# Kernel tuning notes

Hardware: AMD Instinct MI355X
Metric: run time of the kernel (lower is better)

The kernel has to match this reference:

```python
import jax, jax.numpy as jnp
import numpy as np

U, I, E = 50000, 100000, 1600000
D, H, HID, B = 64, 8, 8, 16384
ALPHA = 0.2  # leaky relu slope


def setup_inputs() -> dict:
    key = jax.random.key(0)
    ks = jax.random.split(key, 12)
    return {
        "userIdx": jax.random.randint(ks[0], (B,), 0, U),
        "itemIdx": jax.random.randint(ks[1], (B,), 0, I),
        "edge_u": jax.random.randint(ks[2], (E,), 0, U),
        "edge_i": jax.random.randint(ks[3], (E,), 0, I),
        "uEmbd": jax.random.normal(ks[4], (U, D), dtype=jnp.float32) * 0.01,
        "iEmbd": jax.random.normal(ks[5], (I, D), dtype=jnp.float32) * 0.01,
        "Wu_h": jax.random.normal(ks[6], (H, D, HID), dtype=jnp.float32) * 0.18,
        "Wi_h": jax.random.normal(ks[7], (H, D, HID), dtype=jnp.float32) * 0.18,
        "a_h": jax.random.normal(ks[8], (H, 2 * HID), dtype=jnp.float32) * 0.3,
        "Wu_out": jax.random.normal(ks[9], (H * HID, D), dtype=jnp.float32) * 0.15,
        "Wi_out": jax.random.normal(ks[10], (H * HID, D), dtype=jnp.float32) * 0.15,
        "a_out": jax.random.normal(ks[11], (2 * D,), dtype=jnp.float32) * 0.1,
    }


def _leaky(x):
    return jnp.where(x >= 0, x, ALPHA * x)


def _gat_layer(fu, fi, Wu, Wi, a, edge_u, edge_i):
    # fu:[U,in], fi:[I,in], Wu/Wi:[in,out], a:[2*out]
    u_h = fu @ Wu  # [U,out]
    i_h = fi @ Wi  # [I,out]
    out = Wu.shape[1]
    # a . cat(u_h[eu], i_h[ei]) decomposed into per-node scores then edge gather
    su = u_h @ a[:out]  # [U]
    si = i_h @ a[out:]  # [I]
    e = jnp.exp(-_leaky(su[edge_u] + si[edge_i]))  # [E]
    rowsum = jax.ops.segment_sum(e, edge_u, num_segments=U)  # [U]
    colsum = jax.ops.segment_sum(e, edge_i, num_segments=I)  # [I]
    # users aggregate items they interacted with
    agg_i = jax.ops.segment_sum(e[:, None] * i_h[edge_i], edge_u, num_segments=U)  # [U,out]
    u_p = u_h + agg_i / jnp.where(rowsum == 0, 1.0, rowsum)[:, None]
    # items aggregate users (nan from empty cols -> 0, as in original)
    agg_u = jax.ops.segment_sum(e[:, None] * u_h[edge_u], edge_i, num_segments=I)  # [I,out]
    att_u = jnp.where((colsum > 0)[:, None], agg_u / jnp.where(colsum == 0, 1.0, colsum)[:, None], 0.0)
    i_p = i_h + att_u
    return u_p, i_p


def reference(userIdx, itemIdx, edge_u, edge_i, uEmbd, iEmbd, Wu_h, Wi_h, a_h, Wu_out, Wi_out, a_out):
    # eval mode: all dropout layers are identity
    fu, fi = uEmbd, iEmbd
    head = jax.vmap(lambda Wu, Wi, a: _gat_layer(fu, fi, Wu, Wi, a, edge_u, edge_i))
    u_ps, i_ps = head(Wu_h, Wi_h, a_h)  # [H,U,HID], [H,I,HID]
    # concat=True heads: elu then concatenate along feature dim (head-major columns)
    hu = jax.nn.elu(u_ps).transpose(1, 0, 2).reshape(U, H * HID)
    hi = jax.nn.elu(i_ps).transpose(1, 0, 2).reshape(I, H * HID)
    u_p, i_p = _gat_layer(hu, hi, Wu_out, Wi_out, a_out, edge_u, edge_i)
    u_f = jax.nn.elu(u_p)  # final F.elu in SpUIGAT
    i_f = jax.nn.elu(i_p)
    return jnp.sum(u_f[userIdx] * i_f[itemIdx], axis=1)  # [B]
```

## Files before the change

### kernel.cpp

```cpp
#include <hip/hip_runtime.h>
#include <hip/hip_fp16.h>

#define U_N 50000
#define I_N 100000
#define E_N 1600000
#define B_N 16384
#define UI_N (U_N + I_N)
#define NB_U 782
#define NB_I 1563
#define NBK 586
#define CAP 10240
#define NBLD 512
#define CHUNK (E_N / NBLD)
#define COL_CAP 3300000
#define MAXACT 32768

__global__ __launch_bounds__(1024) void k_build1(
    const int* __restrict__ eu, const int* __restrict__ ei,
    int* __restrict__ bcnt, int* __restrict__ storage) {
  __shared__ int hist[NBK];
  __shared__ int lbase[NBK];
  __shared__ int loff[NBK];
  int t = threadIdx.x;
  for (int b = t; b < NBK; b += 1024) { hist[b] = 0; loff[b] = 0; }
  __syncthreads();
  int e0 = blockIdx.x * CHUNK;
  int myu[4], myi[4];
  int ne = 0;
#pragma unroll
  for (int k = 0; k < 4; k++) {
    int e = e0 + t + 1024 * k;
    if (e < e0 + CHUNK) {
      int u = eu[e], it = ei[e];
      myu[k] = u;
      myi[k] = it;
      ne = k + 1;
      atomicAdd(&hist[u >> 8], 1);
      atomicAdd(&hist[(U_N + it) >> 8], 1);
    }
  }
  __syncthreads();
  for (int b = t; b < NBK; b += 1024) {
    int h = hist[b];
    lbase[b] = h ? atomicAdd(&bcnt[b], h) : 0;
  }
  __syncthreads();
#pragma unroll
  for (int k = 0; k < 4; k++) {
    if (k < ne) {
      int u = myu[k], it = myi[k];
      int k2 = U_N + it;
      int b1 = u >> 8;
      int s1 = lbase[b1] + atomicAdd(&loff[b1], 1);
      storage[(size_t)b1 * CAP + s1] = ((u & 255) << 17) | it;
      int b2 = k2 >> 8;
      int s2 = lbase[b2] + atomicAdd(&loff[b2], 1);
      storage[(size_t)b2 * CAP + s2] = ((k2 & 255) << 17) | u;
    }
  }
}

__global__ __launch_bounds__(1024) void k_scanb(const int* __restrict__ bcnt,
                                                int* __restrict__ bbase) {
  __shared__ int sc[1024];
  int t = threadIdx.x;
  int v = (t < NBK) ? bcnt[t] : 0;
  sc[t] = v;
  __syncthreads();
  int val = v;
  for (int off = 1; off < 1024; off <<= 1) {
    int x = (t >= off) ? sc[t - off] : 0;
    __syncthreads();
    val += x;
    sc[t] = val;
    __syncthreads();
  }
  if (t < NBK) bbase[t] = val - v;
}

__global__ __launch_bounds__(256) void k_build2(const int* __restrict__ bcnt,
                                                const int* __restrict__ storage,
                                                const int* __restrict__ bbase,
                                                int* __restrict__ ptr,
                                                int* __restrict__ col) {
  __shared__ int c[256];
  __shared__ int sc[256];
  __shared__ int pb[256];
  __shared__ int cur[256];
  int b = blockIdx.x;
  int t = threadIdx.x;
  c[t] = 0;
  __syncthreads();
  int n = bcnt[b];
  const int* s = storage + (size_t)b * CAP;
  for (int i = t; i < n; i += 256) atomicAdd(&c[s[i] >> 17], 1);
  __syncthreads();
  int deg = c[t];
  sc[t] = deg;
  __syncthreads();
  int val = deg;
  for (int off = 1; off < 256; off <<= 1) {
    int x = (t >= off) ? sc[t - off] : 0;
    __syncthreads();
    val += x;
    sc[t] = val;
    __syncthreads();
  }
  int base = bbase[b];
  int myPtr = base + (val - deg);
  pb[t] = myPtr;
  cur[t] = 0;
  int node = b * 256 + t;
  if (node < UI_N) ptr[node] = myPtr;
  if (b == NBK - 1 && t == 255) ptr[UI_N] = base + val;
  __syncthreads();
  for (int i = t; i < n; i += 256) {
    int e = s[i];
    int local = e >> 17;
    int slot = pb[local] + atomicAdd(&cur[local], 1);
    col[slot] = e & 0x1FFFF;
  }
}

__global__ void k_flagc(const int* __restrict__ uIdx, const int* __restrict__ iIdx,
                        int* __restrict__ flag, int* __restrict__ list,
                        int* __restrict__ nm) {
  int b = blockIdx.x * blockDim.x + threadIdx.x;
  if (b < B_N) {
    int u = uIdx[b];
    if (atomicExch(&flag[u], 1) == 0) list[atomicAdd(nm, 1)] = u;
    int it = U_N + iIdx[b];
    if (atomicExch(&flag[it], 1) == 0) list[atomicAdd(nm, 1)] = it;
  }
}

__global__ __launch_bounds__(256) void k_mm2(
    const float* __restrict__ Xu32, const float* __restrict__ Xi32,
    const __half* __restrict__ Xu16, const __half* __restrict__ Xi16,
    const float* __restrict__ Wu, const float* __restrict__ Wi,
    const float* __restrict__ a, int layer,
    __half* __restrict__ fA_U, __half* __restrict__ fA_I,
    __half* __restrict__ s16U, __half* __restrict__ s16I) {
  __shared__ float Wl[4096];
  __shared__ float Xs[4096];
  const bool isU = blockIdx.x < NB_U;
  const int N = isU ? U_N : I_N;
  const int base = (isU ? blockIdx.x : blockIdx.x - NB_U) * 64;
  const float* W = isU ? Wu : Wi;
  __half* f16 = isU ? fA_U : fA_I;
  __half* s16 = isU ? s16U : s16I;
  const int aoff = (layer == 1) ? (isU ? 0 : 8) : (isU ? 0 : 64);
  int t = threadIdx.x;

  if (layer == 1) {
#pragma unroll
    for (int k = 0; k < 4; k++) {
      int i = t + 256 * k;
      int h = i >> 7, d = (i >> 1) & 63, half = i & 1;
      float4 v = *(const float4*)(W + h * 512 + d * 8 + half * 4);
      *(float4*)(Wl + d * 64 + h * 8 + half * 4) = v;
    }
    const float* X = isU ? Xu32 : Xi32;
#pragma unroll
    for (int k = 0; k < 4; k++) {
      int i = t + 256 * k;
      int r = i >> 4, ch = i & 15;
      int node = base + r;
      float4 v = make_float4(0.f, 0.f, 0.f, 0.f);
      if (node < N) v = *(const float4*)(X + (size_t)node * 64 + ch * 4);
      *(float4*)(Xs + r * 64 + ch * 4) = v;
    }
  } else {
#pragma unroll
    for (int k = 0; k < 4; k++) {
      int i = t + 256 * k;
      *(float4*)(Wl + i * 4) = *(const float4*)(W + i * 4);
    }
    const __half* X = isU ? Xu16 : Xi16;
#pragma unroll
    for (int k = 0; k < 4; k++) {
      int i = t + 256 * k;
      int r = i >> 4, ch = i & 15;
      int node = base + r;
      float4 v = make_float4(0.f, 0.f, 0.f, 0.f);
      if (node < N) {
        const __half2* hp = (const __half2*)(X + (size_t)node * 64 + ch * 4);
        float2 f0 = __half22float2(hp[0]);
        float2 f1 = __half22float2(hp[1]);
        v = make_float4(f0.x, f0.y, f1.x, f1.y);
      }
      *(float4*)(Xs + r * 64 + ch * 4) = v;
    }
  }
  __syncthreads();

  const int c0 = t & 31;
  const int rb = t >> 5;
  float acc0[8], acc1[8];
#pragma unroll
  for (int k = 0; k < 8; k++) { acc0[k] = 0.f; acc1[k] = 0.f; }

  for (int d0 = 0; d0 < 64; d0 += 4) {
    float2 wA = *(float2*)(Wl + (d0 + 0) * 64 + 2 * c0);
    float2 wB = *(float2*)(Wl + (d0 + 1) * 64 + 2 * c0);
    float2 wC = *(float2*)(Wl + (d0 + 2) * 64 + 2 * c0);
    float2 wD = *(float2*)(Wl + (d0 + 3) * 64 + 2 * c0);
#pragma unroll
    for (int k = 0; k < 8; k++) {
      float4 x = *(float4*)(Xs + (rb + 8 * k) * 64 + d0);
      acc0[k] += x.x * wA.x + x.y * wB.x + x.z * wC.x + x.w * wD.x;
      acc1[k] += x.x * wA.y + x.y * wB.y + x.z * wC.y + x.w * wD.y;
    }
  }

  float av0, av1;
  if (layer == 1) {
    int h = c0 >> 2, j = 2 * (c0 & 3);
    av0 = a[h * 16 + aoff + j];
    av1 = a[h * 16 + aoff + j + 1];
  } else {
    av0 = a[aoff + 2 * c0];
    av1 = a[aoff + 2 * c0 + 1];
  }
#pragma unroll
  for (int k = 0; k < 8; k++) {
    int node = base + rb + 8 * k;
    float s = acc0[k] * av0 + acc1[k] * av1;
    s += __shfl_xor(s, 1);
    s += __shfl_xor(s, 2);
    if (layer != 1) {
      s += __shfl_xor(s, 4);
      s += __shfl_xor(s, 8);
      s += __shfl_xor(s, 16);
    }
    if (node < N) {
      float2 f;
      f.x = acc0[k];
      f.y = acc1[k];
      *(__half2*)(f16 + (size_t)node * 64 + 2 * c0) = __float22half2_rn(f);
      if (layer == 1) {
        if ((c0 & 3) == 0) s16[node * 8 + (c0 >> 2)] = __float2half_rn(s);
      } else {
        if (c0 == 0) s16[node] = __float2half_rn(s);
      }
    }
  }
}

template <int LAYER>
__device__ __forceinline__ void agg_body(
    const int* __restrict__ ptr, const int* __restrict__ col,
    const __half* __restrict__ fA_U, const __half* __restrict__ fA_I,
    __half* __restrict__ fB_U, __half* __restrict__ fB_I,
    const __half* __restrict__ s16U, const __half* __restrict__ s16I,
    const int* __restrict__ list, const int* __restrict__ nm) {
  int gid = blockIdx.x * blockDim.x + threadIdx.x;
  int wv = gid >> 6;
  int l = threadIdx.x & 63;
  int half = l >> 5;
  int idx = wv * 2 + half;
  bool act = true;
  int n;
  if (LAYER == 2) {
    act = idx < *nm;
    n = act ? list[idx] : 0;
  } else {
    n = idx;
  }
  int lh = l & 31;
  int g = lh >> 3;
  int cc = lh & 7;
  bool isU = n < U_N;
  int nl = isU ? n : n - U_N;
  const char* nbrF = (const char*)(isU ? fA_I : fA_U);
  const char* nbrS = (const char*)(isU ? s16I : s16U);
  const __half* selfS = isU ? s16U : s16I;
  const __half* selfF = isU ? fA_U : fA_I;
  __half* outp = isU ? fB_U : fB_I;
  const char* colc = (const char*)col;

  int beg = ptr[n], endA = ptr[n + 1];
  int deg = act ? (endA - beg) : 0;
  unsigned coff = ((unsigned)(beg + g)) << 2;
  const unsigned begb = (unsigned)beg << 2;
  const unsigned fsh = (unsigned)cc << 4;
  const unsigned ssh = (LAYER == 1) ? ((unsigned)cc << 1) : 0u;
  float sself = (LAYER == 1) ? __half2float(selfS[(size_t)nl * 8 + cc])
                             : __half2float(selfS[nl]);
  float acc[8];
#pragma unroll
  for (int k = 0; k < 8; k++) acc[k] = 0.f;
  float wsum = 0.f;

  auto edge = [&](unsigned off) {
    int nb = *(const int*)(colc + off);
    unsigned so = (LAYER == 1) ? (((unsigned)nb << 4) + ssh) : ((unsigned)nb << 1);
    float x = sself + __half2float(*(const __half*)(nbrS + so));
    float4 r = *(const float4*)(nbrF + (((unsigned)nb << 7) + fsh));
    float w = __expf(-fmaxf(x, 0.2f * x));
    wsum += w;
    const __half* h = (const __half*)&r;
#pragma unroll
    for (int k = 0; k < 8; k++) acc[k] += w * (float)h[k];
  };
  auto edgem = [&](unsigned off, bool valid) {
    unsigned o = valid ? off : begb;
    int nb = *(const int*)(colc + o);
    unsigned so = (LAYER == 1) ? (((unsigned)nb << 4) + ssh) : ((unsigned)nb << 1);
    float x = sself + __half2float(*(const __half*)(nbrS + so));
    float4 r = *(const float4*)(nbrF + (((unsigned)nb << 7) + fsh));
    float w = valid ? __expf(-fmaxf(x, 0.2f * x)) : 0.f;
    wsum += w;
    const __half* h = (const __half*)&r;
#pragma unroll
    for (int k = 0; k < 8; k++) acc[k] += w * (float)h[k];
  };

  int q = deg >> 4;
  for (; q > 0; q--) {
    edge(coff);
    edge(coff + 16);
    edge(coff + 32);
    edge(coff + 48);
    coff += 64;
  }
  int rem = deg & 15;
  if (rem) {
    edgem(coff, g < rem);
    edgem(coff + 16, (4 + g) < rem);
    edgem(coff + 32, (8 + g) < rem);
    edgem(coff + 48, (12 + g) < rem);
  }

#pragma unroll
  for (int k = 0; k < 8; k++) {
    acc[k] += __shfl_xor(acc[k], 8);
    acc[k] += __shfl_xor(acc[k], 16);
  }
  wsum += __shfl_xor(wsum, 8);
  wsum += __shfl_xor(wsum, 16);

  if (lh < 8 && act) {
    float4 raw = *(const float4*)(selfF + (size_t)nl * 64 + cc * 8);
    const __half2* sp = (const __half2*)&raw;
    float2 s0 = __half22float2(sp[0]);
    float2 s1 = __half22float2(sp[1]);
    float2 s2 = __half22float2(sp[2]);
    float2 s3 = __half22float2(sp[3]);
    float v[8] = {s0.x, s0.y, s1.x, s1.y, s2.x, s2.y, s3.x, s3.y};
    if (deg > 0) {
      float inv = 1.f / wsum;
#pragma unroll
      for (int k = 0; k < 8; k++) v[k] += acc[k] * inv;
    }
#pragma unroll
    for (int k = 0; k < 8; k++) v[k] = (v[k] > 0.f) ? v[k] : (__expf(v[k]) - 1.f);
    __half2 o[4];
    o[0] = __floats2half2_rn(v[0], v[1]);
    o[1] = __floats2half2_rn(v[2], v[3]);
    o[2] = __floats2half2_rn(v[4], v[5]);
    o[3] = __floats2half2_rn(v[6], v[7]);
    *(float4*)(outp + (size_t)nl * 64 + cc * 8) = *(float4*)o;
  }
}

__global__ __launch_bounds__(256) void k_aggL1(
    const int* __restrict__ ptr, const int* __restrict__ col,
    const __half* __restrict__ fA_U, const __half* __restrict__ fA_I,
    __half* __restrict__ fB_U, __half* __restrict__ fB_I,
    const __half* __restrict__ s16U, const __half* __restrict__ s16I) {
  agg_body<1>(ptr, col, fA_U, fA_I, fB_U, fB_I, s16U, s16I, nullptr, nullptr);
}

__global__ __launch_bounds__(256) void k_aggL2(
    const int* __restrict__ ptr, const int* __restrict__ col,
    const __half* __restrict__ fA_U, const __half* __restrict__ fA_I,
    __half* __restrict__ fB_U, __half* __restrict__ fB_I,
    const __half* __restrict__ s2U, const __half* __restrict__ s2I,
    const int* __restrict__ list, const int* __restrict__ nm) {
  agg_body<2>(ptr, col, fA_U, fA_I, fB_U, fB_I, s2U, s2I, list, nm);
}

__global__ void k_dot(const int* __restrict__ uIdx, const int* __restrict__ iIdx,
                      const __half* __restrict__ u_f, const __half* __restrict__ i_f,
                      float* __restrict__ out) {
  int t = threadIdx.x;
  int pair = blockIdx.x * 32 + (t >> 3);
  int cc = t & 7;
  float4 ra = *(const float4*)(u_f + (size_t)uIdx[pair] * 64 + cc * 8);
  float4 rb = *(const float4*)(i_f + (size_t)iIdx[pair] * 64 + cc * 8);
  const __half* ha = (const __half*)&ra;
  const __half* hb = (const __half*)&rb;
  float v = 0.f;
#pragma unroll
  for (int k = 0; k < 8; k++) v += (float)ha[k] * (float)hb[k];
  v += __shfl_xor(v, 1);
  v += __shfl_xor(v, 2);
  v += __shfl_xor(v, 4);
  if (cc == 0) out[pair] = v;
}

extern "C" void kernel_launch(void* const* d_in, const int* in_sizes, int n_in,
                              void* d_out, int out_size, void* d_ws, size_t ws_size,
                              hipStream_t stream) {
  const int* userIdx = (const int*)d_in[0];
  const int* itemIdx = (const int*)d_in[1];
  const int* edge_u = (const int*)d_in[2];
  const int* edge_i = (const int*)d_in[3];
  const float* uEmbd = (const float*)d_in[4];
  const float* iEmbd = (const float*)d_in[5];
  const float* Wu_h = (const float*)d_in[6];
  const float* Wi_h = (const float*)d_in[7];
  const float* a_h = (const float*)d_in[8];
  const float* Wu_out = (const float*)d_in[9];
  const float* Wi_out = (const float*)d_in[10];
  const float* a_out = (const float*)d_in[11];
  float* out = (float*)d_out;

  char* w = (char*)d_ws;
  size_t off = 0;
  auto alloc = [&](size_t bytes) -> void* {
    void* p = w + off;
    off += (bytes + 511) & ~(size_t)511;
    return p;
  };
  int* bcnt = (int*)alloc((size_t)(NBK + 16 + UI_N) * 4);
  int* nm = bcnt + NBK;
  int* flag = bcnt + NBK + 16;
  int* ptr = (int*)alloc((size_t)(UI_N + 1) * 4);
  int* bbase = (int*)alloc(4096);
  int* list = (int*)alloc((size_t)MAXACT * 4);
  int* col = (int*)alloc((size_t)COL_CAP * 4);
  __half* fA_U = (__half*)alloc((size_t)U_N * 64 * 2);
  __half* fA_I = (__half*)alloc((size_t)I_N * 64 * 2);
  __half* s16U = (__half*)alloc((size_t)U_N * 8 * 2);
  __half* s16I = (__half*)alloc((size_t)I_N * 8 * 2);
  __half* s2U = (__half*)alloc((size_t)U_N * 2);
  __half* s2I = (__half*)alloc((size_t)I_N * 2);
  size_t union_off = off;
  int* storage = (int*)alloc((size_t)NBK * CAP * 4);
  size_t end_storage = off;
  off = union_off;
  __half* fB_U = (__half*)alloc((size_t)U_N * 64 * 2);
  __half* fB_I = (__half*)alloc((size_t)I_N * 64 * 2);
  if (off < end_storage) off = end_storage;

  hipMemsetAsync(bcnt, 0, (size_t)(NBK + 16 + UI_N) * 4, stream);
  k_build1<<<NBLD, 1024, 0, stream>>>(edge_u, edge_i, bcnt, storage);
  k_scanb<<<1, 1024, 0, stream>>>(bcnt, bbase);
  k_build2<<<NBK, 256, 0, stream>>>(bcnt, storage, bbase, ptr, col);
  k_flagc<<<(B_N + 255) / 256, 256, 0, stream>>>(userIdx, itemIdx, flag, list, nm);

  k_mm2<<<NB_U + NB_I, 256, 0, stream>>>(uEmbd, iEmbd, (const __half*)nullptr,
                                         (const __half*)nullptr, Wu_h, Wi_h, a_h, 1,
                                         fA_U, fA_I, s16U, s16I);
  k_aggL1<<<UI_N * 32 / 256, 256, 0, stream>>>(ptr, col, fA_U, fA_I, fB_U, fB_I,
                                               s16U, s16I);

  k_mm2<<<NB_U + NB_I, 256, 0, stream>>>((const float*)nullptr, (const float*)nullptr,
                                         fB_U, fB_I, Wu_out, Wi_out, a_out, 2,
                                         fA_U, fA_I, s2U, s2I);
  k_aggL2<<<MAXACT * 32 / 256, 256, 0, stream>>>(ptr, col, fA_U, fA_I, fB_U, fB_I,
                                                 s2U, s2I, list, nm);

  k_dot<<<B_N / 32, 256, 0, stream>>>(userIdx, itemIdx, fB_U, fB_I, out);
}
```

Measured before the change: 305.8 us.

## Fuse CSR build, flag, and layer-1 matmul into one launch; unify node arrays

Removes the single-block scan kernel. Each build2 block now computes its own base by summing the preceding bucket counts, and build2, the flag pass and the layer-1 matmul run as block ranges of one fused kernel. Node features and scores move into unified user+item arrays with global column indices, which removes the user/item pointer selection inside the aggregation. The tail edges use predicated calls instead of masked dummy loads, and every lane now writes a slice of the epilogue instead of only eight lanes. The cost is a redundant prefix sum in every build2 block (up to 585 reads each), and the matmul blocks in the fused launch do not depend on the CSR build.

```diff
diff --git a/kernel.cpp b/kernel.cpp
--- a/kernel.cpp
+++ b/kernel.cpp
@@ -52,61 +52,49 @@
       int k2 = U_N + it;
       int b1 = u >> 8;
       int s1 = lbase[b1] + atomicAdd(&loff[b1], 1);
-      storage[(size_t)b1 * CAP + s1] = ((u & 255) << 17) | it;
+      storage[(size_t)b1 * CAP + s1] = ((u & 255) << 18) | k2;
       int b2 = k2 >> 8;
       int s2 = lbase[b2] + atomicAdd(&loff[b2], 1);
-      storage[(size_t)b2 * CAP + s2] = ((k2 & 255) << 17) | u;
-    }
-  }
-}
-
-__global__ __launch_bounds__(1024) void k_scanb(const int* __restrict__ bcnt,
-                                                int* __restrict__ bbase) {
-  __shared__ int sc[1024];
+      storage[(size_t)b2 * CAP + s2] = ((k2 & 255) << 18) | u;
+    }
+  }
+}
+
+__device__ void build2_body(int b, const int* __restrict__ bcnt,
+                            const int* __restrict__ storage,
+                            int* __restrict__ ptr, int* __restrict__ col,
+                            int* smem) {
+  int* c = smem;
+  int* sc = smem + 256;
+  int* pb = smem + 512;
+  int* cur = smem + 768;
   int t = threadIdx.x;
-  int v = (t < NBK) ? bcnt[t] : 0;
-  sc[t] = v;
-  __syncthreads();
-  int val = v;
-  for (int off = 1; off < 1024; off <<= 1) {
-    int x = (t >= off) ? sc[t - off] : 0;
+  int pre = 0;
+  for (int i = t; i < b; i += 256) pre += bcnt[i];
+  sc[t] = pre;
+  c[t] = 0;
+  __syncthreads();
+  for (int o = 128; o > 0; o >>= 1) {
+    if (t < o) sc[t] += sc[t + o];
+    __syncthreads();
+  }
+  int base = sc[0];
+  __syncthreads();
+  int n = bcnt[b];
+  const int* s = storage + (size_t)b * CAP;
+  for (int i = t; i < n; i += 256) atomicAdd(&c[s[i] >> 18], 1);
+  __syncthreads();
+  int deg = c[t];
+  sc[t] = deg;
+  __syncthreads();
+  int val = deg;
+  for (int o = 1; o < 256; o <<= 1) {
+    int x = (t >= o) ? sc[t - o] : 0;
     __syncthreads();
     val += x;
     sc[t] = val;
     __syncthreads();
   }
-  if (t < NBK) bbase[t] = val - v;
-}
-
-__global__ __launch_bounds__(256) void k_build2(const int* __restrict__ bcnt,
-                                                const int* __restrict__ storage,
-                                                const int* __restrict__ bbase,
-                                                int* __restrict__ ptr,
-                                                int* __restrict__ col) {
-  __shared__ int c[256];
-  __shared__ int sc[256];
-  __shared__ int pb[256];
-  __shared__ int cur[256];
-  int b = blockIdx.x;
-  int t = threadIdx.x;
-  c[t] = 0;
-  __syncthreads();
-  int n = bcnt[b];
-  const int* s = storage + (size_t)b * CAP;
-  for (int i = t; i < n; i += 256) atomicAdd(&c[s[i] >> 17], 1);
-  __syncthreads();
-  int deg = c[t];
-  sc[t] = deg;
-  __syncthreads();
-  int val = deg;
-  for (int off = 1; off < 256; off <<= 1) {
-    int x = (t >= off) ? sc[t - off] : 0;
-    __syncthreads();
-    val += x;
-    sc[t] = val;
-    __syncthreads();
-  }
-  int base = bbase[b];
   int myPtr = base + (val - deg);
   pb[t] = myPtr;
   cur[t] = 0;
@@ -116,16 +104,17 @@
   __syncthreads();
   for (int i = t; i < n; i += 256) {
     int e = s[i];
-    int local = e >> 17;
+    int local = e >> 18;
     int slot = pb[local] + atomicAdd(&cur[local], 1);
-    col[slot] = e & 0x1FFFF;
-  }
-}
-
-__global__ void k_flagc(const int* __restrict__ uIdx, const int* __restrict__ iIdx,
-                        int* __restrict__ flag, int* __restrict__ list,
-                        int* __restrict__ nm) {
-  int b = blockIdx.x * blockDim.x + threadIdx.x;
+    col[slot] = e & 0x3FFFF;
+  }
+}
+
+__device__ __forceinline__ void flagc_body(int bid, const int* __restrict__ uIdx,
+                                           const int* __restrict__ iIdx,
+                                           int* __restrict__ flag, int* __restrict__ list,
+                                           int* __restrict__ nm) {
+  int b = bid * 256 + threadIdx.x;
   if (b < B_N) {
     int u = uIdx[b];
     if (atomicExch(&flag[u], 1) == 0) list[atomicAdd(nm, 1)] = u;
@@ -134,21 +123,19 @@
   }
 }
 
-__global__ __launch_bounds__(256) void k_mm2(
-    const float* __restrict__ Xu32, const float* __restrict__ Xi32,
-    const __half* __restrict__ Xu16, const __half* __restrict__ Xi16,
+__device__ __forceinline__ void mm2_body(
+    int bid, const float* __restrict__ Xu32, const float* __restrict__ Xi32,
+    const __half* __restrict__ X16,
     const float* __restrict__ Wu, const float* __restrict__ Wi,
     const float* __restrict__ a, int layer,
-    __half* __restrict__ fA_U, __half* __restrict__ fA_I,
-    __half* __restrict__ s16U, __half* __restrict__ s16I) {
-  __shared__ float Wl[4096];
-  __shared__ float Xs[4096];
-  const bool isU = blockIdx.x < NB_U;
+    __half* __restrict__ f16,
+    __half* __restrict__ s16,
+    float* Wl, float* Xs) {
+  const bool isU = bid < NB_U;
   const int N = isU ? U_N : I_N;
-  const int base = (isU ? blockIdx.x : blockIdx.x - NB_U) * 64;
+  const int base = (isU ? bid : bid - NB_U) * 64;
+  const int gofs = isU ? 0 : U_N;
   const float* W = isU ? Wu : Wi;
-  __half* f16 = isU ? fA_U : fA_I;
-  __half* s16 = isU ? s16U : s16I;
   const int aoff = (layer == 1) ? (isU ? 0 : 8) : (isU ? 0 : 64);
   int t = threadIdx.x;
 
@@ -176,7 +163,6 @@
       int i = t + 256 * k;
       *(float4*)(Wl + i * 4) = *(const float4*)(W + i * 4);
     }
-    const __half* X = isU ? Xu16 : Xi16;
 #pragma unroll
     for (int k = 0; k < 4; k++) {
       int i = t + 256 * k;
@@ -184,7 +170,7 @@
       int node = base + r;
       float4 v = make_float4(0.f, 0.f, 0.f, 0.f);
       if (node < N) {
-        const __half2* hp = (const __half2*)(X + (size_t)node * 64 + ch * 4);
+        const __half2* hp = (const __half2*)(X16 + (size_t)(gofs + node) * 64 + ch * 4);
         float2 f0 = __half22float2(hp[0]);
         float2 f1 = __half22float2(hp[1]);
         v = make_float4(f0.x, f0.y, f1.x, f1.y);
@@ -234,25 +220,55 @@
       s += __shfl_xor(s, 16);
     }
     if (node < N) {
+      int gn = gofs + node;
       float2 f;
       f.x = acc0[k];
       f.y = acc1[k];
-      *(__half2*)(f16 + (size_t)node * 64 + 2 * c0) = __float22half2_rn(f);
+      *(__half2*)(f16 + (size_t)gn * 64 + 2 * c0) = __float22half2_rn(f);
       if (layer == 1) {
-        if ((c0 & 3) == 0) s16[node * 8 + (c0 >> 2)] = __float2half_rn(s);
+        if ((c0 & 3) == 0) s16[gn * 8 + (c0 >> 2)] = __float2half_rn(s);
       } else {
-        if (c0 == 0) s16[node] = __float2half_rn(s);
+        if (c0 == 0) s16[gn] = __float2half_rn(s);
       }
     }
   }
+}
+
+__global__ __launch_bounds__(256) void k_fused2(
+    const int* __restrict__ bcnt, const int* __restrict__ storage,
+    int* __restrict__ ptr, int* __restrict__ col,
+    const int* __restrict__ uIdx, const int* __restrict__ iIdx,
+    int* __restrict__ flag, int* __restrict__ list, int* __restrict__ nm,
+    const float* __restrict__ uEmbd, const float* __restrict__ iEmbd,
+    const float* __restrict__ Wu, const float* __restrict__ Wi,
+    const float* __restrict__ a, __half* __restrict__ fA, __half* __restrict__ s16) {
+  __shared__ float4 smv[2048];
+  int bx = blockIdx.x;
+  if (bx < NBK) {
+    build2_body(bx, bcnt, storage, ptr, col, (int*)smv);
+  } else if (bx < NBK + 64) {
+    flagc_body(bx - NBK, uIdx, iIdx, flag, list, nm);
+  } else {
+    float* s = (float*)smv;
+    mm2_body(bx - NBK - 64, uEmbd, iEmbd, nullptr, Wu, Wi, a, 1, fA, s16, s, s + 4096);
+  }
+}
+
+__global__ __launch_bounds__(256) void k_mm2(
+    const __half* __restrict__ X16, const float* __restrict__ Wu,
+    const float* __restrict__ Wi, const float* __restrict__ a,
+    __half* __restrict__ f16, __half* __restrict__ s2) {
+  __shared__ float4 smv[2048];
+  float* s = (float*)smv;
+  mm2_body(blockIdx.x, nullptr, nullptr, X16, Wu, Wi, a, 2, f16, s2, s, s + 4096);
 }
 
 template <int LAYER>
 __device__ __forceinline__ void agg_body(
     const int* __restrict__ ptr, const int* __restrict__ col,
-    const __half* __restrict__ fA_U, const __half* __restrict__ fA_I,
-    __half* __restrict__ fB_U, __half* __restrict__ fB_I,
-    const __half* __restrict__ s16U, const __half* __restrict__ s16I,
+    const __half* __restrict__ fA,
+    __half* __restrict__ fB,
+    const __half* __restrict__ sc,
     const int* __restrict__ list, const int* __restrict__ nm) {
   int gid = blockIdx.x * blockDim.x + threadIdx.x;
   int wv = gid >> 6;
@@ -270,46 +286,28 @@
   int lh = l & 31;
   int g = lh >> 3;
   int cc = lh & 7;
-  bool isU = n < U_N;
-  int nl = isU ? n : n - U_N;
-  const char* nbrF = (const char*)(isU ? fA_I : fA_U);
-  const char* nbrS = (const char*)(isU ? s16I : s16U);
-  const __half* selfS = isU ? s16U : s16I;
-  const __half* selfF = isU ? fA_U : fA_I;
-  __half* outp = isU ? fB_U : fB_I;
-  const char* colc = (const char*)col;
 
   int beg = ptr[n], endA = ptr[n + 1];
   int deg = act ? (endA - beg) : 0;
   unsigned coff = ((unsigned)(beg + g)) << 2;
-  const unsigned begb = (unsigned)beg << 2;
   const unsigned fsh = (unsigned)cc << 4;
   const unsigned ssh = (LAYER == 1) ? ((unsigned)cc << 1) : 0u;
-  float sself = (LAYER == 1) ? __half2float(selfS[(size_t)nl * 8 + cc])
-                             : __half2float(selfS[nl]);
+  float sself = (LAYER == 1) ? __half2float(sc[(size_t)n * 8 + cc])
+                             : __half2float(sc[n]);
   float acc[8];
 #pragma unroll
   for (int k = 0; k < 8; k++) acc[k] = 0.f;
   float wsum = 0.f;
+  const char* colc = (const char*)col;
+  const char* fAc = (const char*)fA;
+  const char* scc = (const char*)sc;
 
   auto edge = [&](unsigned off) {
     int nb = *(const int*)(colc + off);
     unsigned so = (LAYER == 1) ? (((unsigned)nb << 4) + ssh) : ((unsigned)nb << 1);
-    float x = sself + __half2float(*(const __half*)(nbrS + so));
-    float4 r = *(const float4*)(nbrF + (((unsigned)nb << 7) + fsh));
+    float x = sself + __half2float(*(const __half*)(scc + so));
+    float4 r = *(const float4*)(fAc + (((unsigned)nb << 7) + fsh));
     float w = __expf(-fmaxf(x, 0.2f * x));
-    wsum += w;
-    const __half* h = (const __half*)&r;
-#pragma unroll
-    for (int k = 0; k < 8; k++) acc[k] += w * (float)h[k];
-  };
-  auto edgem = [&](unsigned off, bool valid) {
-    unsigned o = valid ? off : begb;
-    int nb = *(const int*)(colc + o);
-    unsigned so = (LAYER == 1) ? (((unsigned)nb << 4) + ssh) : ((unsigned)nb << 1);
-    float x = sself + __half2float(*(const __half*)(nbrS + so));
-    float4 r = *(const float4*)(nbrF + (((unsigned)nb << 7) + fsh));
-    float w = valid ? __expf(-fmaxf(x, 0.2f * x)) : 0.f;
     wsum += w;
     const __half* h = (const __half*)&r;
 #pragma unroll
@@ -326,10 +324,10 @@
   }
   int rem = deg & 15;
   if (rem) {
-    edgem(coff, g < rem);
-    edgem(coff + 16, (4 + g) < rem);
-    edgem(coff + 32, (8 + g) < rem);
-    edgem(coff + 48, (12 + g) < rem);
+    if (g < rem) edge(coff);
+    if (g + 4 < rem) edge(coff + 16);
+    if (g + 8 < rem) edge(coff + 32);
+    if (g + 12 < rem) edge(coff + 48);
   }
 
 #pragma unroll
@@ -340,45 +338,36 @@
   wsum += __shfl_xor(wsum, 8);
   wsum += __shfl_xor(wsum, 16);
 
-  if (lh < 8 && act) {
-    float4 raw = *(const float4*)(selfF + (size_t)nl * 64 + cc * 8);
-    const __half2* sp = (const __half2*)&raw;
-    float2 s0 = __half22float2(sp[0]);
-    float2 s1 = __half22float2(sp[1]);
-    float2 s2 = __half22float2(sp[2]);
-    float2 s3 = __half22float2(sp[3]);
-    float v[8] = {s0.x, s0.y, s1.x, s1.y, s2.x, s2.y, s3.x, s3.y};
-    if (deg > 0) {
-      float inv = 1.f / wsum;
-#pragma unroll
-      for (int k = 0; k < 8; k++) v[k] += acc[k] * inv;
-    }
-#pragma unroll
-    for (int k = 0; k < 8; k++) v[k] = (v[k] > 0.f) ? v[k] : (__expf(v[k]) - 1.f);
-    __half2 o[4];
-    o[0] = __floats2half2_rn(v[0], v[1]);
-    o[1] = __floats2half2_rn(v[2], v[3]);
-    o[2] = __floats2half2_rn(v[4], v[5]);
-    o[3] = __floats2half2_rn(v[6], v[7]);
-    *(float4*)(outp + (size_t)nl * 64 + cc * 8) = *(float4*)o;
+  if (act) {
+    float inv = (deg > 0) ? 1.f / wsum : 0.f;
+    float a0, a1;
+    if (g == 0) { a0 = acc[0]; a1 = acc[1]; }
+    else if (g == 1) { a0 = acc[2]; a1 = acc[3]; }
+    else if (g == 2) { a0 = acc[4]; a1 = acc[5]; }
+    else { a0 = acc[6]; a1 = acc[7]; }
+    size_t boff = (size_t)n * 64 + cc * 8 + 2 * g;
+    float2 sf = __half22float2(*(const __half2*)(fA + boff));
+    float v0 = sf.x + a0 * inv;
+    float v1 = sf.y + a1 * inv;
+    v0 = (v0 > 0.f) ? v0 : (__expf(v0) - 1.f);
+    v1 = (v1 > 0.f) ? v1 : (__expf(v1) - 1.f);
+    *(__half2*)(fB + boff) = __floats2half2_rn(v0, v1);
   }
 }
 
 __global__ __launch_bounds__(256) void k_aggL1(
     const int* __restrict__ ptr, const int* __restrict__ col,
-    const __half* __restrict__ fA_U, const __half* __restrict__ fA_I,
-    __half* __restrict__ fB_U, __half* __restrict__ fB_I,
-    const __half* __restrict__ s16U, const __half* __restrict__ s16I) {
-  agg_body<1>(ptr, col, fA_U, fA_I, fB_U, fB_I, s16U, s16I, nullptr, nullptr);
+    const __half* __restrict__ fA, __half* __restrict__ fB,
+    const __half* __restrict__ s16) {
+  agg_body<1>(ptr, col, fA, fB, s16, nullptr, nullptr);
 }
 
 __global__ __launch_bounds__(256) void k_aggL2(
     const int* __restrict__ ptr, const int* __restrict__ col,
-    const __half* __restrict__ fA_U, const __half* __restrict__ fA_I,
-    __half* __restrict__ fB_U, __half* __restrict__ fB_I,
-    const __half* __restrict__ s2U, const __half* __restrict__ s2I,
-    const int* __restrict__ list, const int* __restrict__ nm) {
-  agg_body<2>(ptr, col, fA_U, fA_I, fB_U, fB_I, s2U, s2I, list, nm);
+    const __half* __restrict__ fA, __half* __restrict__ fB,
+    const __half* __restrict__ s2, const int* __restrict__ list,
+    const int* __restrict__ nm) {
+  agg_body<2>(ptr, col, fA, fB, s2, list, nm);
 }
 
 __global__ void k_dot(const int* __restrict__ uIdx, const int* __restrict__ iIdx,
@@ -428,40 +417,29 @@
   int* nm = bcnt + NBK;
   int* flag = bcnt + NBK + 16;
   int* ptr = (int*)alloc((size_t)(UI_N + 1) * 4);
-  int* bbase = (int*)alloc(4096);
   int* list = (int*)alloc((size_t)MAXACT * 4);
   int* col = (int*)alloc((size_t)COL_CAP * 4);
-  __half* fA_U = (__half*)alloc((size_t)U_N * 64 * 2);
-  __half* fA_I = (__half*)alloc((size_t)I_N * 64 * 2);
-  __half* s16U = (__half*)alloc((size_t)U_N * 8 * 2);
-  __half* s16I = (__half*)alloc((size_t)I_N * 8 * 2);
-  __half* s2U = (__half*)alloc((size_t)U_N * 2);
-  __half* s2I = (__half*)alloc((size_t)I_N * 2);
+  __half* fA = (__half*)alloc((size_t)UI_N * 64 * 2);
+  __half* s16 = (__half*)alloc((size_t)UI_N * 8 * 2);
+  __half* s2 = (__half*)alloc((size_t)UI_N * 2);
   size_t union_off = off;
   int* storage = (int*)alloc((size_t)NBK * CAP * 4);
   size_t end_storage = off;
   off = union_off;
-  __half* fB_U = (__half*)alloc((size_t)U_N * 64 * 2);
-  __half* fB_I = (__half*)alloc((size_t)I_N * 64 * 2);
+  __half* fB = (__half*)alloc((size_t)UI_N * 64 * 2);
   if (off < end_storage) off = end_storage;
 
   hipMemsetAsync(bcnt, 0, (size_t)(NBK + 16 + UI_N) * 4, stream);
   k_build1<<<NBLD, 1024, 0, stream>>>(edge_u, edge_i, bcnt, storage);
-  k_scanb<<<1, 1024, 0, stream>>>(bcnt, bbase);
-  k_build2<<<NBK, 256, 0, stream>>>(bcnt, storage, bbase, ptr, col);
-  k_flagc<<<(B_N + 255) / 256, 256, 0, stream>>>(userIdx, itemIdx, flag, list, nm);
-
-  k_mm2<<<NB_U + NB_I, 256, 0, stream>>>(uEmbd, iEmbd, (const __half*)nullptr,
-                                         (const __half*)nullptr, Wu_h, Wi_h, a_h, 1,
-                                         fA_U, fA_I, s16U, s16I);
-  k_aggL1<<<UI_N * 32 / 256, 256, 0, stream>>>(ptr, col, fA_U, fA_I, fB_U, fB_I,
-                                               s16U, s16I);
-
-  k_mm2<<<NB_U + NB_I, 256, 0, stream>>>((const float*)nullptr, (const float*)nullptr,
-                                         fB_U, fB_I, Wu_out, Wi_out, a_out, 2,
-                                         fA_U, fA_I, s2U, s2I);
-  k_aggL2<<<MAXACT * 32 / 256, 256, 0, stream>>>(ptr, col, fA_U, fA_I, fB_U, fB_I,
-                                                 s2U, s2I, list, nm);
-
-  k_dot<<<B_N / 32, 256, 0, stream>>>(userIdx, itemIdx, fB_U, fB_I, out);
-}
+
+  k_fused2<<<NBK + 64 + NB_U + NB_I, 256, 0, stream>>>(
+      bcnt, storage, ptr, col, userIdx, itemIdx, flag, list, nm,
+      uEmbd, iEmbd, Wu_h, Wi_h, a_h, fA, s16);
+
+  k_aggL1<<<UI_N * 32 / 256, 256, 0, stream>>>(ptr, col, fA, fB, s16);
+
+  k_mm2<<<NB_U + NB_I, 256, 0, stream>>>(fB, Wu_out, Wi_out, a_out, fA, s2);
+  k_aggL2<<<MAXACT * 32 / 256, 256, 0, stream>>>(ptr, col, fA, fB, s2, list, nm);
+
+  k_dot<<<B_N / 32, 256, 0, stream>>>(userIdx, itemIdx, fB, fB + (size_t)U_N * 64, out);
+}
```

Result: faster. 288.5 us (-5.7%).
